# Kernel optimization log

Hardware: AMD Instinct MI355X
Metric: run time of the kernel (lower is better)

The kernel has to match this reference:

```python
import jax, jax.numpy as jnp
import numpy as np

DIM = 1024
D_INNER = 1024
D_STATE = 2048


def setup_inputs() -> dict:
    key = jax.random.key(0)
    ks = jax.random.split(key, 6)
    Bsz, T = 8, 2048
    x = jax.random.normal(ks[0], (Bsz, T, DIM), dtype=jnp.float32)
    h0 = jnp.zeros((Bsz, D_STATE), dtype=jnp.float32)
    # parameters (mamba2_init: normal std=0.02, log_A = 0)
    W_in = jax.random.normal(ks[1], (2 * D_INNER, DIM), dtype=jnp.float32) * 0.02   # nn.Linear weight [out,in]
    W_out = jax.random.normal(ks[2], (DIM, D_INNER), dtype=jnp.float32) * 0.02
    B_mat = jax.random.normal(ks[3], (D_INNER, D_STATE), dtype=jnp.float32) * 0.02
    C_mat = jax.random.normal(ks[4], (D_STATE, D_INNER), dtype=jnp.float32) * 0.02
    log_A = jnp.zeros((D_STATE,), dtype=jnp.float32)
    return {"x": x, "h0": h0, "W_in": W_in, "W_out": W_out,
            "B_mat": B_mat, "C_mat": C_mat, "log_A": log_A}


def reference(x, h0, W_in, W_out, B_mat, C_mat, log_A):
    # x: [B, T, dim]
    xz = jnp.einsum('btd,ed->bte', x, W_in)          # [B, T, 2*d_inner]
    x_proj, z = jnp.split(xz, 2, axis=-1)
    x_proj = jax.nn.silu(x_proj)
    A = jax.nn.sigmoid(log_A)                         # [d_state], fixed (non-selective)

    x_t = jnp.swapaxes(x_proj, 0, 1)                  # [T, B, d_inner]
    z_t = jnp.swapaxes(z, 0, 1)                       # [T, B, d_inner]

    def step(h, xz_t):
        xt, zt = xz_t
        h_new = jnp.tanh(A * h + xt @ B_mat)          # [B, d_state]
        y = (h_new @ C_mat) * jax.nn.silu(zt)         # [B, d_inner]
        return h_new, y

    h_final, y_seq = jax.lax.scan(step, h0, (x_t, z_t))  # y_seq: [T, B, d_inner]
    y = jnp.swapaxes(y_seq, 0, 1)                     # [B, T, d_inner]
    output = jnp.einsum('bti,oi->bto', y, W_out)      # [B, T, dim]
    return output, h_final
```

## Files before the change

kernel.cpp:

```cpp
#include <hip/hip_runtime.h>
#include <cstdint>
#include <cstddef>

#define DIM    1024
#define DINNER 1024
#define DSTATE 2048
#define BSZ    8
#define TLEN   2048
#define MROWS  (BSZ * TLEN)

typedef unsigned short u16;
typedef __attribute__((ext_vector_type(8))) __bf16 bf16x8;
typedef __attribute__((ext_vector_type(4))) float  f32x4;
typedef __attribute__((ext_vector_type(8))) u16    u16x8;

static __device__ __forceinline__ u16 f2bf(float f) {
  union { float f; uint32_t u; } v; v.f = f;
  uint32_t u = v.u;
  return (u16)((u + 0x7fffu + ((u >> 16) & 1u)) >> 16);
}

static __device__ __forceinline__ float bf2f(u16 b) {
  union { uint32_t u; float f; } v; v.u = ((uint32_t)b) << 16;
  return v.f;
}

static __device__ __forceinline__ float silu(float x) {
  return x / (1.f + __expf(-x));
}

__global__ void sentinel(float* out) { out[0] = 12345.0f; }


__global__ void cast_bf16x8(const float* __restrict__ in, u16* __restrict__ out, long n) {
  long i = ((long)blockIdx.x * blockDim.x + threadIdx.x) * 8;
  if (i >= n) return;
  float4 a = *(const float4*)(in + i);
  float4 b = *(const float4*)(in + i + 4);
  u16x8 o;
  o[0] = f2bf(a.x); o[1] = f2bf(a.y); o[2] = f2bf(a.z); o[3] = f2bf(a.w);
  o[4] = f2bf(b.x); o[5] = f2bf(b.y); o[6] = f2bf(b.z); o[7] = f2bf(b.w);
  *(u16x8*)(out + i) = o;
}

__global__ void transpose_cast(const float* __restrict__ in, u16* __restrict__ out,
                               int R, int C) {
  __shared__ float t[32][33];
  int c0 = blockIdx.x * 32, r0 = blockIdx.y * 32;
  int tx = threadIdx.x, ty = threadIdx.y;
#pragma unroll
  for (int i = 0; i < 32; i += 8)
    t[ty + i][tx] = in[(size_t)(r0 + ty + i) * C + c0 + tx];
  __syncthreads();
#pragma unroll
  for (int i = 0; i < 32; i += 8)
    out[(size_t)(c0 + ty + i) * R + r0 + tx] = f2bf(t[tx][ty + i]);
}


#define SEG  128
#define WARM 32

__global__ void __launch_bounds__(256) winscan(const u16* __restrict__ xB,
                                               u16* __restrict__ H,
                                               const float* __restrict__ h0,
                                               const float* __restrict__ logA,
                                               float* __restrict__ hf,
                                               int b0) {
  const int NSEG = TLEN / SEG;
  int tid  = blockIdx.x * 256 + threadIdx.x;
  int s    = tid & (DSTATE - 1);
  int rest = tid >> 11;
  int bl   = rest >> 4;
  int seg  = rest & (NSEG - 1);

  const float C2  = 2.8853900817779268f;
  const float L2E = 1.4426950408889634f;
  float A  = __builtin_amdgcn_rcpf(1.f + __builtin_amdgcn_exp2f(-logA[s] * L2E));
  float Ac = A * C2;

  const int t0 = seg * SEG;
  float h;
  const u16* src;
  if (seg == 0) {
    h = h0[(size_t)(b0 + bl) * DSTATE + s];
    src = xB + ((size_t)bl * TLEN) * DSTATE + s;
  } else {
    h = 0.f;
    src = xB + ((size_t)bl * TLEN + (t0 - WARM)) * DSTATE + s;
#pragma unroll
    for (int i = 0; i < WARM; ++i) {
      float g = fmaf(Ac, h, bf2f(src[(size_t)i * DSTATE]) * C2);
      float e = __builtin_amdgcn_exp2f(g);
      float r = __builtin_amdgcn_rcpf(e + 1.f);
      h = fmaf(-2.f, r, 1.f);
    }
    src += (size_t)WARM * DSTATE;
  }

  u16* dst = H + ((size_t)bl * TLEN + t0) * DSTATE + s;
  const int PF = 8;
  float buf[PF], nbuf[PF];
#pragma unroll
  for (int i = 0; i < PF; ++i) buf[i] = bf2f(src[(size_t)i * DSTATE]) * C2;
  for (int tc = 0; tc < SEG; tc += PF) {
    if (tc + PF < SEG) {
#pragma unroll
      for (int i = 0; i < PF; ++i) nbuf[i] = bf2f(src[(size_t)(tc + PF + i) * DSTATE]) * C2;
    }
#pragma unroll
    for (int i = 0; i < PF; ++i) {
      float g = fmaf(Ac, h, buf[i]);
      float e = __builtin_amdgcn_exp2f(g);
      float r = __builtin_amdgcn_rcpf(e + 1.f);
      h = fmaf(-2.f, r, 1.f);
      dst[(size_t)(tc + i) * DSTATE] = f2bf(h);
    }
#pragma unroll
    for (int i = 0; i < PF; ++i) buf[i] = nbuf[i];
  }
  if (seg == NSEG - 1) hf[(size_t)(b0 + bl) * DSTATE + s] = h;
}


enum { EPI_F32 = 0, EPI_SILU_SPLIT = 1, EPI_BF16 = 2, EPI_MUL_SZ = 3 };

#define GBAR()  __builtin_amdgcn_s_barrier()
#define LGKM0() do { asm volatile("s_waitcnt lgkmcnt(0)" ::: "memory"); \
                     __builtin_amdgcn_sched_barrier(0); } while (0)

template <int EPI>
__global__ void __launch_bounds__(512, 2) gemm256(const u16* __restrict__ A,
                                                  const u16* __restrict__ B,
                                                  float* __restrict__ Cf,
                                                  u16* __restrict__ O1,
                                                  u16* __restrict__ O2,
                                                  const u16* __restrict__ SZ,
                                                  int M, int N, int K) {
  extern __shared__ u16 lds[];
  const int tid = threadIdx.x, wid = tid >> 6, lane = tid & 63;
  const int wm = wid >> 2, wn = wid & 3;

  int bx = blockIdx.x, by = blockIdx.y;
  {
    int gx = gridDim.x, gy = gridDim.y;
    int nwg = gx * gy;
    int wg  = blockIdx.y * gx + blockIdx.x;
    if ((nwg & 7) == 0) {
      int v = (wg & 7) * (nwg >> 3) + (wg >> 3);
      bx = v / gy;
      by = v - bx * gy;
    }
  }
  const int m0 = bx * 256, n0 = by * 256;

  const int fr = lane & 15;
  const int kbs8 = ((lane >> 4) ^ ((fr >> 1) & 3)) * 8;
  const int srow = tid >> 2, skb = tid & 3;

  f32x4 acc[8][4] = {};
  bf16x8 af[8], bfj[4];

  auto STG = [&](int db, int mat, int ks, int kt) {
#pragma unroll
    for (int c = 0; c < 2; ++c) {
      int row = c * 128 + srow;
      int ksrc8 = (skb ^ ((row >> 1) & 3)) * 8;
      const u16* P = mat ? B : A;
      const u16* g = P + (size_t)((mat ? n0 : m0) + row) * K + (kt << 6) + (ks << 5) + ksrc8;
      u16* d = lds + (((db * 2 + mat) * 2 + ks) << 13) + (c << 12) + (wid << 9);
      __builtin_amdgcn_global_load_lds((const __attribute__((address_space(1))) void*)g,
          (__attribute__((address_space(3))) void*)d, 16, 0, 0);
    }
  };
  auto LDA = [&](int db, int ks) {
    const u16* base = lds + (((db * 2 + 0) * 2 + ks) << 13) + (wm * 128 + fr) * 32 + kbs8;
#pragma unroll
    for (int i = 0; i < 8; ++i) af[i] = *(const bf16x8*)(base + i * 512);
  };
  auto LDB4 = [&](int db, int ks) {
    const u16* base = lds + (((db * 2 + 1) * 2 + ks) << 13) + (wn * 64 + fr) * 32 + kbs8;
#pragma unroll
    for (int j = 0; j < 4; ++j) bfj[j] = *(const bf16x8*)(base + j * 512);
  };
  auto MM = [&](int jp) {
    __builtin_amdgcn_s_setprio(1);
#pragma unroll
    for (int i = 0; i < 8; ++i) {
      acc[i][jp * 2]     = __builtin_amdgcn_mfma_f32_16x16x32_bf16(af[i], bfj[jp * 2],     acc[i][jp * 2],     0, 0, 0);
      acc[i][jp * 2 + 1] = __builtin_amdgcn_mfma_f32_16x16x32_bf16(af[i], bfj[jp * 2 + 1], acc[i][jp * 2 + 1], 0, 0, 0);
    }
    __builtin_amdgcn_s_setprio(0);
  };

  const int T = K >> 6;
  const int I = T >> 1;

  STG(0, 0, 0, 0); STG(0, 1, 0, 0); STG(0, 0, 1, 0); STG(0, 1, 1, 0);
  STG(1, 0, 0, 1); STG(1, 1, 0, 1); STG(1, 0, 1, 1);
  asm volatile("s_waitcnt vmcnt(6)" ::: "memory");

  for (int it = 0; it < I; ++it) {
    const bool last = (it == I - 1);
    const int t1 = 2 * it + 1, t2 = 2 * it + 2, t3 = 2 * it + 3;

    GBAR(); STG(1, 1, 1, t1); LDA(0, 0); LDB4(0, 0);
    LGKM0(); MM(0);
    GBAR(); if (!last) STG(0, 0, 0, t2); MM(1);

    GBAR(); if (!last) STG(0, 1, 0, t2); LDA(0, 1); LDB4(0, 1);
    LGKM0(); MM(0);
    GBAR(); if (!last) STG(0, 0, 1, t2);
    if (last) { asm volatile("s_waitcnt vmcnt(0)" ::: "memory"); }
    else      { asm volatile("s_waitcnt vmcnt(6)" ::: "memory"); }
    MM(1);

    GBAR(); if (!last) STG(0, 1, 1, t2); LDA(1, 0); LDB4(1, 0);
    LGKM0(); MM(0);
    GBAR(); if (!last) STG(1, 0, 0, t3); MM(1);

    GBAR(); if (!last) STG(1, 1, 0, t3); LDA(1, 1); LDB4(1, 1);
    LGKM0(); MM(0);
    GBAR();
    if (!last) { STG(1, 0, 1, t3); asm volatile("s_waitcnt vmcnt(6)" ::: "memory"); }
    MM(1);
  }
  GBAR();

  {
    float* esl = (float*)lds + wid * (16 * 66);
    const int cr = (lane >> 4) * 4;
    const int cc = lane & 15;
    const int erow = lane >> 2;
    const int ecol = (lane & 3) * 16;
#pragma unroll
    for (int i = 0; i < 8; ++i) {
#pragma unroll
      for (int j = 0; j < 4; ++j)
#pragma unroll
        for (int r = 0; r < 4; ++r)
          esl[(cr + r) * 66 + j * 16 + cc] = acc[i][j][r];
      asm volatile("s_waitcnt lgkmcnt(0)" ::: "memory");
      __builtin_amdgcn_sched_barrier(0);
      f32x4 v0 = *(const f32x4*)(esl + erow * 66 + ecol);
      f32x4 v1 = *(const f32x4*)(esl + erow * 66 + ecol + 4);
      f32x4 v2 = *(const f32x4*)(esl + erow * 66 + ecol + 8);
      f32x4 v3 = *(const f32x4*)(esl + erow * 66 + ecol + 12);
      asm volatile("s_waitcnt lgkmcnt(0)" ::: "memory");
      __builtin_amdgcn_sched_barrier(0);
      const int gm = m0 + wm * 128 + i * 16 + erow;
      const int gn = n0 + wn * 64 + ecol;
      if constexpr (EPI == EPI_F32) {
        float* cp = Cf + (size_t)gm * N + gn;
        *(f32x4*)(cp)      = v0;
        *(f32x4*)(cp + 4)  = v1;
        *(f32x4*)(cp + 8)  = v2;
        *(f32x4*)(cp + 12) = v3;
      } else if constexpr (EPI == EPI_BF16) {
        u16x8 o1, o2;
#pragma unroll
        for (int r = 0; r < 4; ++r) { o1[r] = f2bf(v0[r]); o1[4 + r] = f2bf(v1[r]); }
#pragma unroll
        for (int r = 0; r < 4; ++r) { o2[r] = f2bf(v2[r]); o2[4 + r] = f2bf(v3[r]); }
        u16* op = O1 + (size_t)gm * N + gn;
        *(u16x8*)(op) = o1;
        *(u16x8*)(op + 8) = o2;
      } else if constexpr (EPI == EPI_SILU_SPLIT) {
        u16x8 o1, o2;
#pragma unroll
        for (int r = 0; r < 4; ++r) { o1[r] = f2bf(silu(v0[r])); o1[4 + r] = f2bf(silu(v1[r])); }
#pragma unroll
        for (int r = 0; r < 4; ++r) { o2[r] = f2bf(silu(v2[r])); o2[4 + r] = f2bf(silu(v3[r])); }
        const int half = N >> 1;
        u16* op = (gn < half ? O1 + (size_t)gm * half + gn
                             : O2 + (size_t)gm * half + (gn - half));
        *(u16x8*)(op) = o1;
        *(u16x8*)(op + 8) = o2;
      } else {
        const u16* sp = SZ + (size_t)gm * N + gn;
        u16x8 s1 = *(const u16x8*)(sp);
        u16x8 s2 = *(const u16x8*)(sp + 8);
        u16x8 o1, o2;
#pragma unroll
        for (int r = 0; r < 4; ++r) { o1[r] = f2bf(v0[r] * bf2f(s1[r])); o1[4 + r] = f2bf(v1[r] * bf2f(s1[4 + r])); }
#pragma unroll
        for (int r = 0; r < 4; ++r) { o2[r] = f2bf(v2[r] * bf2f(s2[r])); o2[4 + r] = f2bf(v3[r] * bf2f(s2[4 + r])); }
        u16* op = O1 + (size_t)gm * N + gn;
        *(u16x8*)(op) = o1;
        *(u16x8*)(op + 8) = o2;
      }
    }
  }
}


extern "C" void kernel_launch(void* const* d_in, const int* in_sizes, int n_in,
                              void* d_out, int out_size, void* d_ws, size_t ws_size,
                              hipStream_t stream) {
  const float* x     = (const float*)d_in[0];
  const float* h0    = (const float*)d_in[1];
  const float* W_in  = (const float*)d_in[2];
  const float* W_out = (const float*)d_in[3];
  const float* Bm    = (const float*)d_in[4];
  const float* Cm    = (const float*)d_in[5];
  const float* logA  = (const float*)d_in[6];
  float* out = (float*)d_out;
  float* hf  = out + (size_t)MROWS * DIM;

  const int LDSB = 131072;
  hipFuncSetAttribute((const void*)gemm256<EPI_F32>,        hipFuncAttributeMaxDynamicSharedMemorySize, LDSB);
  hipFuncSetAttribute((const void*)gemm256<EPI_SILU_SPLIT>, hipFuncAttributeMaxDynamicSharedMemorySize, LDSB);
  hipFuncSetAttribute((const void*)gemm256<EPI_BF16>,       hipFuncAttributeMaxDynamicSharedMemorySize, LDSB);
  hipFuncSetAttribute((const void*)gemm256<EPI_MUL_SZ>,     hipFuncAttributeMaxDynamicSharedMemorySize, LDSB);

  auto align256 = [](size_t b) { return (b + 255) & ~(size_t)255; };

  const size_t w_win  = align256((size_t)2 * DINNER * DIM * 2);
  const size_t w_wout = align256((size_t)DIM * DINNER * 2);
  const size_t w_bt   = align256((size_t)DSTATE * DINNER * 2);
  const size_t w_ct   = align256((size_t)DINNER * DSTATE * 2);
  const size_t w_weights = w_win + w_wout + w_bt + w_ct;

  int nb = 0;
  const int cand[4] = {8, 4, 2, 1};
  size_t su = 0, sx = 0, ssz = 0, sxb = 0;
  for (int ci = 0; ci < 4; ++ci) {
    int c = cand[ci];
    size_t Mc = (size_t)c * TLEN;
    su  = (size_t)Mc * DINNER * 2;
    sx  = (size_t)Mc * DINNER * 2;
    ssz = (size_t)Mc * DINNER * 2;
    sxb = (size_t)Mc * DSTATE * 2;
    if (w_weights + su + sx + ssz + sxb <= ws_size) { nb = c; break; }
  }
  if (!nb) { sentinel<<<1, 1, 0, stream>>>(out); return; }

  char* ws = (char*)d_ws;
  u16* Win_bf  = (u16*)ws;             ws += w_win;
  u16* Wout_bf = (u16*)ws;             ws += w_wout;
  u16* BT_bf   = (u16*)ws;             ws += w_bt;
  u16* CT_bf   = (u16*)ws;             ws += w_ct;
  u16* u_bf    = (u16*)ws;             ws += su;
  u16* x_bf    = (u16*)ws;             ws += sx;
  u16* sz_bf   = (u16*)ws;             ws += ssz;
  u16* xB_bf   = (u16*)ws;             ws += sxb;
  u16* H_bf    = u_bf;
  u16* y_bf    = xB_bf;

  cast_bf16x8<<<(2 * DINNER * DIM) / 8 / 256, 256, 0, stream>>>(W_in, Win_bf, (long)2 * DINNER * DIM);
  cast_bf16x8<<<(DIM * DINNER) / 8 / 256, 256, 0, stream>>>(W_out, Wout_bf, (long)DIM * DINNER);
  transpose_cast<<<dim3(DSTATE / 32, DINNER / 32), dim3(32, 8), 0, stream>>>(Bm, BT_bf, DINNER, DSTATE);
  transpose_cast<<<dim3(DINNER / 32, DSTATE / 32), dim3(32, 8), 0, stream>>>(Cm, CT_bf, DSTATE, DINNER);

  for (int b0 = 0; b0 < BSZ; b0 += nb) {
    const int Mc = nb * TLEN;
    const float* xc = x + (size_t)b0 * TLEN * DIM;
    float* outc = out + (size_t)b0 * TLEN * DIM;

    cast_bf16x8<<<((size_t)Mc * DIM) / 8 / 256, 256, 0, stream>>>(xc, x_bf, (long)Mc * DIM);

    gemm256<EPI_SILU_SPLIT><<<dim3(Mc / 256, (2 * DINNER) / 256), 512, LDSB, stream>>>(
        x_bf, Win_bf, nullptr, u_bf, sz_bf, nullptr, Mc, 2 * DINNER, DIM);

    gemm256<EPI_BF16><<<dim3(Mc / 256, DSTATE / 256), 512, LDSB, stream>>>(
        u_bf, BT_bf, nullptr, xB_bf, nullptr, nullptr, Mc, DSTATE, DINNER);

    winscan<<<Mc / 16, 256, 0, stream>>>(xB_bf, H_bf, h0, logA, hf, b0);

    gemm256<EPI_MUL_SZ><<<dim3(Mc / 256, DINNER / 256), 512, LDSB, stream>>>(
        H_bf, CT_bf, nullptr, y_bf, nullptr, sz_bf, Mc, DINNER, DSTATE);

    gemm256<EPI_F32><<<dim3(Mc / 256, DIM / 256), 512, LDSB, stream>>>(
        y_bf, Wout_bf, outc, nullptr, nullptr, nullptr, Mc, DIM, DINNER);
  }
}
```

Before: 339.1 us.

## Load GEMM B fragments directly from global into registers, stage only A in LDS

The 256x256 GEMM kernel no longer stages the B tile through LDS. Each wave now loads its B fragments straight from global memory into double-buffered registers (bf0/bf1), one k-slice ahead of use. Only A goes through LDS, and the epilogue scratch is moved past the A buffers, which shrinks the LDS footprint and halves LDS traffic per step. In exchange, the four wn-waves sharing a column re-read the same B data from global/L2, and register pressure rises from the extra fragment buffer.

```diff
diff --git a/kernel.cpp b/kernel.cpp
--- a/kernel.cpp
+++ b/kernel.cpp
@@ -155,80 +155,69 @@
   const int m0 = bx * 256, n0 = by * 256;
 
   const int fr = lane & 15;
-  const int kbs8 = ((lane >> 4) ^ ((fr >> 1) & 3)) * 8;
+  const int kb = lane >> 4;
+  const int kbs8 = (kb ^ ((fr >> 1) & 3)) * 8;
   const int srow = tid >> 2, skb = tid & 3;
 
   f32x4 acc[8][4] = {};
-  bf16x8 af[8], bfj[4];
-
-  auto STG = [&](int db, int mat, int ks, int kt) {
+  bf16x8 af[8], bf0[4], bf1[4];
+
+  auto STG = [&](int db, int ks, int kt) {
 #pragma unroll
     for (int c = 0; c < 2; ++c) {
       int row = c * 128 + srow;
       int ksrc8 = (skb ^ ((row >> 1) & 3)) * 8;
-      const u16* P = mat ? B : A;
-      const u16* g = P + (size_t)((mat ? n0 : m0) + row) * K + (kt << 6) + (ks << 5) + ksrc8;
-      u16* d = lds + (((db * 2 + mat) * 2 + ks) << 13) + (c << 12) + (wid << 9);
+      const u16* g = A + (size_t)(m0 + row) * K + (kt << 6) + (ks << 5) + ksrc8;
+      u16* d = lds + ((db * 2 + ks) << 13) + (c << 12) + (wid << 9);
       __builtin_amdgcn_global_load_lds((const __attribute__((address_space(1))) void*)g,
           (__attribute__((address_space(3))) void*)d, 16, 0, 0);
     }
   };
   auto LDA = [&](int db, int ks) {
-    const u16* base = lds + (((db * 2 + 0) * 2 + ks) << 13) + (wm * 128 + fr) * 32 + kbs8;
+    const u16* base = lds + ((db * 2 + ks) << 13) + (wm * 128 + fr) * 32 + kbs8;
 #pragma unroll
     for (int i = 0; i < 8; ++i) af[i] = *(const bf16x8*)(base + i * 512);
   };
-  auto LDB4 = [&](int db, int ks) {
-    const u16* base = lds + (((db * 2 + 1) * 2 + ks) << 13) + (wn * 64 + fr) * 32 + kbs8;
-#pragma unroll
-    for (int j = 0; j < 4; ++j) bfj[j] = *(const bf16x8*)(base + j * 512);
+  const u16* Bg = B + (size_t)(n0 + wn * 64 + fr) * K + kb * 8;
+  auto BLD = [&](bf16x8* bf, int kt, int ks) {
+#pragma unroll
+    for (int j = 0; j < 4; ++j)
+      bf[j] = *(const bf16x8*)(Bg + (size_t)j * 16 * K + (kt << 6) + (ks << 5));
   };
-  auto MM = [&](int jp) {
+  auto MM = [&](const bf16x8* bf) {
     __builtin_amdgcn_s_setprio(1);
 #pragma unroll
-    for (int i = 0; i < 8; ++i) {
-      acc[i][jp * 2]     = __builtin_amdgcn_mfma_f32_16x16x32_bf16(af[i], bfj[jp * 2],     acc[i][jp * 2],     0, 0, 0);
-      acc[i][jp * 2 + 1] = __builtin_amdgcn_mfma_f32_16x16x32_bf16(af[i], bfj[jp * 2 + 1], acc[i][jp * 2 + 1], 0, 0, 0);
-    }
+    for (int i = 0; i < 8; ++i)
+#pragma unroll
+      for (int j = 0; j < 4; ++j)
+        acc[i][j] = __builtin_amdgcn_mfma_f32_16x16x32_bf16(af[i], bf[j], acc[i][j], 0, 0, 0);
     __builtin_amdgcn_s_setprio(0);
   };
 
   const int T = K >> 6;
   const int I = T >> 1;
 
-  STG(0, 0, 0, 0); STG(0, 1, 0, 0); STG(0, 0, 1, 0); STG(0, 1, 1, 0);
-  STG(1, 0, 0, 1); STG(1, 1, 0, 1); STG(1, 0, 1, 1);
-  asm volatile("s_waitcnt vmcnt(6)" ::: "memory");
+  STG(0, 0, 0); STG(0, 1, 0); STG(1, 0, 1);
+  BLD(bf0, 0, 0);
+  asm volatile("s_waitcnt vmcnt(8)" ::: "memory");
 
   for (int it = 0; it < I; ++it) {
     const bool last = (it == I - 1);
-    const int t1 = 2 * it + 1, t2 = 2 * it + 2, t3 = 2 * it + 3;
-
-    GBAR(); STG(1, 1, 1, t1); LDA(0, 0); LDB4(0, 0);
-    LGKM0(); MM(0);
-    GBAR(); if (!last) STG(0, 0, 0, t2); MM(1);
-
-    GBAR(); if (!last) STG(0, 1, 0, t2); LDA(0, 1); LDB4(0, 1);
-    LGKM0(); MM(0);
-    GBAR(); if (!last) STG(0, 0, 1, t2);
-    if (last) { asm volatile("s_waitcnt vmcnt(0)" ::: "memory"); }
-    else      { asm volatile("s_waitcnt vmcnt(6)" ::: "memory"); }
-    MM(1);
-
-    GBAR(); if (!last) STG(0, 1, 1, t2); LDA(1, 0); LDB4(1, 0);
-    LGKM0(); MM(0);
-    GBAR(); if (!last) STG(1, 0, 0, t3); MM(1);
-
-    GBAR(); if (!last) STG(1, 1, 0, t3); LDA(1, 1); LDB4(1, 1);
-    LGKM0(); MM(0);
-    GBAR();
-    if (!last) { STG(1, 0, 1, t3); asm volatile("s_waitcnt vmcnt(6)" ::: "memory"); }
-    MM(1);
+    const int t0 = 2 * it, t1 = 2 * it + 1, t2 = 2 * it + 2, t3 = 2 * it + 3;
+
+    GBAR(); STG(1, 1, t1); BLD(bf1, t0, 1);
+    LDA(0, 0); LGKM0(); MM(bf0);
+    GBAR(); if (!last) STG(0, 0, t2); BLD(bf0, t1, 0);
+    LDA(0, 1); LGKM0(); MM(bf1);
+    GBAR(); if (!last) STG(0, 1, t2); BLD(bf1, t1, 1);
+    LDA(1, 0); LGKM0(); MM(bf0);
+    GBAR(); if (!last) { STG(1, 0, t3); BLD(bf0, t2, 0); }
+    LDA(1, 1); LGKM0(); MM(bf1);
   }
   GBAR();
 
   {
-    float* esl = (float*)lds + wid * (16 * 66);
+    float* esl = (float*)(lds + 32768) + wid * (16 * 66);
     const int cr = (lane >> 4) * 4;
     const int cc = lane & 15;
     const int erow = lane >> 2;
@@ -307,7 +296,7 @@
   float* out = (float*)d_out;
   float* hf  = out + (size_t)MROWS * DIM;
 
-  const int LDSB = 131072;
+  const int LDSB = 65536 + 33792;
   hipFuncSetAttribute((const void*)gemm256<EPI_F32>,        hipFuncAttributeMaxDynamicSharedMemorySize, LDSB);
   hipFuncSetAttribute((const void*)gemm256<EPI_SILU_SPLIT>, hipFuncAttributeMaxDynamicSharedMemorySize, LDSB);
   hipFuncSetAttribute((const void*)gemm256<EPI_BF16>,       hipFuncAttributeMaxDynamicSharedMemorySize, LDSB);
```

New measurement: 442.7 us. 1.31x slower.
